# Kernel tuning notes

Measured on AMD Instinct MI355X. Metric: run time of the kernel, lower is better.

## Reference

```python
import jax, jax.numpy as jnp
import numpy as np

NUM_LAYERS = 4
D_MODEL = 1024
N_HEAD = 8
HEAD_DIM = D_MODEL // N_HEAD
FFN_DIM = 4096
B, L = 8, 512
LN_EPS = 1e-5


def rel_pos_embed(seq_len, dim, init_size=1200, padding_idx=0):
    # RelativeSinusoidalPositionalEmbedding.get_embedding(init_size+1, dim, 0)
    num = init_size + 1  # 1201
    half = dim // 2
    inv = np.exp(np.arange(half, dtype=np.float64) * -(np.log(10000.0) / (half - 1)))
    pos = np.arange(-num // 2, num // 2, dtype=np.float64)[:, None] * inv[None, :]
    emb = np.concatenate([np.sin(pos), np.cos(pos)], axis=1)  # [num, dim]
    emb[padding_idx] = 0.0
    origin_shift = num // 2 + 1  # 601
    idx = np.arange(-seq_len, seq_len) + origin_shift  # [2L]
    return jnp.asarray(emb[idx], dtype=jnp.float32)  # [2L, dim]


def _shift(BD):
    # [b,h,L,2L] -> [b,h,L,L], selecting relative offsets k-q
    b, h, l, _ = BD.shape
    BD = jnp.concatenate([BD, jnp.zeros((b, h, l, 1), BD.dtype)], axis=-1)
    BD = BD.reshape(b, h, -1, l)[:, :, :-1].reshape(b, h, l, 2 * l)
    return BD[:, :, :, l:]


def _transpose_shift(E):
    # [b,h,L,2L] -> [b,h,L,L]
    b, h, l, _ = E.shape
    E = jnp.concatenate([E, jnp.zeros((b, h, l, 1), E.dtype)], axis=-1)
    E = E.reshape(b, h, 2 * l + 1, l)
    E = E[:, :, 2 * jnp.arange(l) + 1, :]  # [b,h,L,L]
    return jnp.swapaxes(E, -1, -2)


def layer_norm(x, g, b):
    mu = x.mean(-1, keepdims=True)
    var = ((x - mu) ** 2).mean(-1, keepdims=True)
    return (x - mu) / jnp.sqrt(var + LN_EPS) * g + b


def rel_attn(x, mask, qkv_w, r_r, r_w, pos):
    bsz, l, d = x.shape
    qkv = x @ qkv_w  # [b,L,3D]
    q, k, v = jnp.split(qkv, 3, axis=-1)
    to_heads = lambda t: t.reshape(bsz, l, N_HEAD, HEAD_DIM).transpose(0, 2, 1, 3)
    q, k, v = to_heads(q), to_heads(k), to_heads(v)  # [b,h,L,hd]
    rw_q = q + r_r[:, None]  # (original adds r_r_bias here)
    AC = jnp.einsum('bnqd,bnkd->bnqk', rw_q, k)
    D_ = jnp.einsum('nd,ld->nl', r_w, pos)[None, :, None]   # [1,h,1,2L]
    B_ = jnp.einsum('bnqd,ld->bnql', q, pos)                # [b,h,L,2L]
    E_ = jnp.einsum('bnqd,ld->bnql', k, pos)
    BDE = _shift(B_ + D_) + _transpose_shift(E_)
    attn = AC + BDE  # scale == 1 (scale=False)
    attn = jnp.where(mask[:, None, None, :] == 0, -jnp.inf, attn)
    attn = jax.nn.softmax(attn, axis=-1)
    out = jnp.einsum('bnqk,bnkd->bnqd', attn, v)
    return out.transpose(0, 2, 1, 3).reshape(bsz, l, d)


def setup_inputs() -> dict:
    key = jax.random.key(0)
    ks = jax.random.split(key, 12)
    Ln = NUM_LAYERS
    s = 0.02
    return {
        'x': jax.random.normal(ks[0], (B, L, D_MODEL), jnp.float32),
        'mask': jnp.ones((B, L), jnp.int32),
        'qkv_w': jax.random.normal(ks[1], (Ln, D_MODEL, 3 * D_MODEL), jnp.float32) * s,
        'r_r_bias': jax.random.normal(ks[2], (Ln, N_HEAD, HEAD_DIM), jnp.float32) * s,
        'r_w_bias': jax.random.normal(ks[3], (Ln, N_HEAD, HEAD_DIM), jnp.float32) * s,
        'ln1_g': jnp.ones((Ln, D_MODEL), jnp.float32),
        'ln1_b': jnp.zeros((Ln, D_MODEL), jnp.float32),
        'ln2_g': jnp.ones((Ln, D_MODEL), jnp.float32),
        'ln2_b': jnp.zeros((Ln, D_MODEL), jnp.float32),
        'w1': jax.random.normal(ks[4], (Ln, D_MODEL, FFN_DIM), jnp.float32) * s,
        'b1': jnp.zeros((Ln, FFN_DIM), jnp.float32),
        'w2': jax.random.normal(ks[5], (Ln, FFN_DIM, D_MODEL), jnp.float32) * s,
        'b2': jnp.zeros((Ln, D_MODEL), jnp.float32),
    }


def reference(x, mask, qkv_w, r_r_bias, r_w_bias, ln1_g, ln1_b, ln2_g, ln2_b, w1, b1, w2, b2):
    pos = rel_pos_embed(x.shape[1], HEAD_DIM)  # [2L, hd], buffer (detached)
    for i in range(NUM_LAYERS):  # after_norm=True (post-LN)
        a = rel_attn(x, mask, qkv_w[i], r_r_bias[i], r_w_bias[i], pos)
        x = layer_norm(x + a, ln1_g[i], ln1_b[i])
        h = jax.nn.relu(x @ w1[i] + b1[i]) @ w2[i] + b2[i]
        x = layer_norm(x + h, ln2_g[i], ln2_b[i])
    return x
```

## Files before the change

### kernel.cpp

```cpp
#include <hip/hip_runtime.h>

#define SEQ 512
#define DM 1024
#define NH 8
#define HD 128
#define FFN 4096
#define NL 4
#define NB 8

typedef __attribute__((ext_vector_type(8))) _Float16 half8v;
typedef __attribute__((ext_vector_type(8))) unsigned short ushort8v;
typedef __attribute__((ext_vector_type(4))) float float4v;

__device__ __forceinline__ unsigned short f2h(float f) {
  _Float16 h = (_Float16)f;
  return *(unsigned short*)&h;
}
__device__ __forceinline__ float h2f(unsigned short u) {
  _Float16 h = *(_Float16*)&u;
  return (float)h;
}

__global__ void sc_kernel(float* __restrict__ sc) {
  int idx = blockIdx.x * blockDim.x + threadIdx.x;
  int q = idx >> 6, c = idx & 63;
  if (q >= SEQ) return;
  double a = exp(-(double)c * (9.210340371976184 / 63.0));
  double p = (double)q * a;
  sc[q * 128 + c] = (float)sin(p);
  sc[q * 128 + 64 + c] = (float)cos(p);
}

__global__ void cvt_copy(const float* __restrict__ in, float* __restrict__ xout,
                         unsigned short* __restrict__ xh, int n4) {
  int i = blockIdx.x * blockDim.x + threadIdx.x;
  if (i >= n4) return;
  float4 v = ((const float4*)in)[i];
  ((float4*)xout)[i] = v;
  ushort4 u;
  u.x = f2h(v.x); u.y = f2h(v.y); u.z = f2h(v.z); u.w = f2h(v.w);
  ((ushort4*)xh)[i] = u;
}

__global__ __launch_bounds__(256) void transpose_cvt(
    const float* __restrict__ in, unsigned short* __restrict__ out, int K, int N) {
  __shared__ float t[32][33];
  int n0 = blockIdx.x * 32, k0 = blockIdx.y * 32;
  int c = threadIdx.x & 31, r = threadIdx.x >> 5;
#pragma unroll
  for (int i = 0; i < 32; i += 8)
    t[r + i][c] = in[(long long)(k0 + r + i) * N + n0 + c];
  __syncthreads();
#pragma unroll
  for (int i = 0; i < 32; i += 8)
    out[(long long)(n0 + r + i) * K + k0 + c] = f2h(t[c][r + i]);
}

template<int R, int T>
__device__ __forceinline__ void stage_tile(
    const unsigned short* __restrict__ g, long long ld, int k0,
    unsigned short* lds, int tid) {
#pragma unroll
  for (int i = 0; i < R * 64 / 8 / T; i++) {
    int p = i * T + tid;
    int row = p >> 3, cs = p & 7;
    int c = cs ^ (row & 7);
    const unsigned short* src = g + (long long)row * ld + k0 + c * 8;
    __builtin_amdgcn_global_load_lds(
        (const __attribute__((address_space(1))) void*)src,
        (__attribute__((address_space(3))) void*)(lds + p * 8),
        16, 0, 0);
  }
}

template<int BIAS, int RELU, int OUTH>
__global__ __launch_bounds__(512, 2) void gemm256(
    const unsigned short* __restrict__ A, int lda, long long sAz,
    const unsigned short* __restrict__ Bt, int ldb, long long sBz,
    const float* __restrict__ bias,
    void* __restrict__ Cv, int ldc, long long sCz,
    int K) {
  __shared__ __align__(16) unsigned short As[2][256 * 64];
  __shared__ __align__(16) unsigned short Bs[2][256 * 64];
  const int tid = threadIdx.x, lane = tid & 63, w = tid >> 6;
  const int wm = w >> 2, wn = w & 3;
  const int l15 = lane & 15, l4 = lane >> 4;
  const int gx = gridDim.x, gy = gridDim.y;
  int nwg = gx * gy * gridDim.z;
  int lin = (blockIdx.z * gy + blockIdx.y) * gx + blockIdx.x;
  int swz = (lin & 7) * (nwg >> 3) + (lin >> 3);
  int bx = swz % gx;
  int t2 = swz / gx;
  int by = t2 % gy;
  int z  = t2 / gy;
  const unsigned short* Ag = A + (long long)z * sAz + (long long)by * 256 * lda;
  const unsigned short* Bg = Bt + (long long)z * sBz + (long long)bx * 256 * ldb;

  float4v acc[8][4] = {};
  const int nt = K >> 6;
  stage_tile<256, 512>(Ag, lda, 0, As[0], tid);
  stage_tile<256, 512>(Bg, ldb, 0, Bs[0], tid);
  int cur = 0;
  for (int t = 0; t < nt; t++) {
    if (t + 1 < nt) {
      stage_tile<256, 512>(Ag, lda, (t + 1) << 6, As[cur ^ 1], tid);
      stage_tile<256, 512>(Bg, ldb, (t + 1) << 6, Bs[cur ^ 1], tid);
      asm volatile("s_waitcnt vmcnt(8)" ::: "memory");
    } else {
      asm volatile("s_waitcnt vmcnt(0)" ::: "memory");
    }
    asm volatile("s_barrier" ::: "memory");
#pragma unroll
    for (int ks = 0; ks < 2; ks++) {
      half8v af[8], bf[4];
#pragma unroll
      for (int m = 0; m < 8; m++) {
        int row = wm * 128 + m * 16 + l15;
        int cs = (ks * 4 + l4) ^ (row & 7);
        af[m] = *(const half8v*)&As[cur][row * 64 + cs * 8];
      }
#pragma unroll
      for (int n = 0; n < 4; n++) {
        int row = wn * 64 + n * 16 + l15;
        int cs = (ks * 4 + l4) ^ (row & 7);
        bf[n] = *(const half8v*)&Bs[cur][row * 64 + cs * 8];
      }
#pragma unroll
      for (int m = 0; m < 8; m++)
#pragma unroll
        for (int n = 0; n < 4; n++)
          acc[m][n] = __builtin_amdgcn_mfma_f32_16x16x32_f16(af[m], bf[n], acc[m][n], 0, 0, 0);
    }
    asm volatile("s_barrier" ::: "memory");
    cur ^= 1;
  }
#pragma unroll
  for (int n = 0; n < 4; n++) {
    int ccol = bx * 256 + wn * 64 + n * 16 + l15;
    float bv = BIAS ? bias[ccol] : 0.f;
#pragma unroll
    for (int m = 0; m < 8; m++) {
      int crow0 = by * 256 + wm * 128 + m * 16 + l4 * 4;
#pragma unroll
      for (int j = 0; j < 4; j++) {
        float v = acc[m][n][j] + bv;
        if (RELU) v = fmaxf(v, 0.f);
        long long off = (long long)z * sCz + (long long)(crow0 + j) * ldc + ccol;
        if (OUTH) ((unsigned short*)Cv)[off] = f2h(v);
        else      ((float*)Cv)[off] = v;
      }
    }
  }
}

__global__ __launch_bounds__(256) void build_aug(
    const unsigned short* __restrict__ qkv_h,
    const float* __restrict__ rr, const float* __restrict__ rw,
    const float* __restrict__ sc,
    unsigned short* __restrict__ Ahat, unsigned short* __restrict__ Bhat)
{
  const int z = blockIdx.y, b = z >> 3, h = z & 7;
  const int r = threadIdx.x >> 7, lane = threadIdx.x & 127;
  const int q = blockIdx.x * 2 + r;
  __shared__ float Qf[2][128], Kf[2][128], SC[2][128];
  const unsigned short* row = qkv_h + ((long long)(b * SEQ + q)) * 3072 + h * HD;
  float qv = h2f(row[lane]);
  float kv = h2f(row[DM + lane]);
  Qf[r][lane] = qv + rw[h * HD + lane];
  Kf[r][lane] = kv;
  SC[r][lane] = sc[q * 128 + lane];
  __syncthreads();
  unsigned short* Arow = Ahat + ((long long)z * SEQ + q) * 384;
  unsigned short* Brow = Bhat + ((long long)z * SEQ + q) * 384;
  Arow[lane] = f2h(qv + rr[h * HD + lane]);
  Brow[lane] = f2h(kv);
  if (lane < 64) {
    float S = SC[r][lane], C = SC[r][64 + lane];
    Arow[128 + lane] = f2h(Qf[r][lane] * C + Qf[r][64 + lane] * S);
    Arow[256 + lane] = f2h(S);
    Brow[128 + lane] = f2h(S);
    Brow[256 + lane] = f2h(Kf[r][lane] * C + Kf[r][64 + lane] * S);
  } else {
    int c = lane - 64;
    float S = SC[r][c], C = SC[r][lane];
    Arow[192 + c] = f2h(Qf[r][lane] * C - Qf[r][c] * S);
    Arow[320 + c] = f2h(C);
    Brow[192 + c] = f2h(C);
    Brow[320 + c] = f2h(Kf[r][lane] * C - Kf[r][c] * S);
  }
}

__global__ __launch_bounds__(256) void transpose_v(
    const unsigned short* __restrict__ qkv_h, unsigned short* __restrict__ Vt)
{
  __shared__ unsigned short t[32][33];
  const int z = blockIdx.z, b = z >> 3, h = z & 7;
  const int d0 = blockIdx.x * 32, j0 = blockIdx.y * 32;
  const int c = threadIdx.x & 31, r = threadIdx.x >> 5;
#pragma unroll
  for (int i = 0; i < 32; i += 8)
    t[r + i][c] = qkv_h[((long long)(b * SEQ + j0 + r + i)) * 3072 + 2 * DM + h * HD + d0 + c];
  __syncthreads();
#pragma unroll
  for (int i = 0; i < 32; i += 8)
    Vt[(long long)z * HD * SEQ + (long long)(d0 + r + i) * SEQ + j0 + c] = t[c][r + i];
}

__global__ __launch_bounds__(512, 4) void attn_fused(
    const unsigned short* __restrict__ Ahat,
    const unsigned short* __restrict__ Bhat,
    const unsigned short* __restrict__ Vt,
    const int* __restrict__ mask,
    unsigned short* __restrict__ out)
{
  __shared__ __align__(16) unsigned short S[64 * 512];
  __shared__ __align__(16) unsigned short St[128 * 64];
  const int tid = threadIdx.x, lane = tid & 63, w = tid >> 6;
  const int wr = w >> 1, wc = w & 1;
  const int l15 = lane & 15, l4 = lane >> 4;
  int lin = blockIdx.z * gridDim.x + blockIdx.x;
  int nwg = gridDim.x * gridDim.z;
  int swz = (lin & 7) * (nwg >> 3) + (lin >> 3);
  int qt = swz % gridDim.x, z = swz / gridDim.x;
  const int b = z >> 3, h = z & 7;
  const int q0 = qt * 64;

  half8v qf[12];
  {
    const unsigned short* Ar = Ahat + ((long long)z * SEQ + q0 + wr * 16 + l15) * 384;
#pragma unroll
    for (int k = 0; k < 12; k++)
      qf[k] = *(const half8v*)&Ar[k * 32 + l4 * 8];
  }

  for (int jt = 0; jt < 4; jt++) {
    float4v acc[4] = {};
    const unsigned short* Bg = Bhat + ((long long)z * SEQ + jt * 128) * 384;
    for (int k0 = 0; k0 < 384; k0 += 64) {
      __syncthreads();
      stage_tile<128, 512>(Bg, 384, k0, St, tid);
      __syncthreads();
#pragma unroll
      for (int kk = 0; kk < 2; kk++) {
        int kidx = (k0 >> 5) + kk;
#pragma unroll
        for (int n = 0; n < 4; n++) {
          int row = wc * 64 + n * 16 + l15;
          int cs = (kk * 4 + l4) ^ (row & 7);
          half8v bf = *(const half8v*)&St[row * 64 + cs * 8];
          acc[n] = __builtin_amdgcn_mfma_f32_16x16x32_f16(qf[kidx], bf, acc[n], 0, 0, 0);
        }
      }
    }
#pragma unroll
    for (int n = 0; n < 4; n++) {
      int col = jt * 128 + wc * 64 + n * 16 + l15;
#pragma unroll
      for (int j = 0; j < 4; j++) {
        int row = wr * 16 + l4 * 4 + j;
        int byte = (row * 512 + col) * 2;
        byte ^= (row & 7) << 4;
        *(unsigned short*)((char*)S + byte) = f2h(acc[n][j]);
      }
    }
  }
  __syncthreads();

  float* bias = (float*)St;
  float* Linv = (float*)St + 512;
  if (tid < 128) {
    int4 mk = ((const int4*)(mask + (size_t)b * SEQ))[tid];
    float4 bv;
    bv.x = mk.x ? 0.f : -1e30f;
    bv.y = mk.y ? 0.f : -1e30f;
    bv.z = mk.z ? 0.f : -1e30f;
    bv.w = mk.w ? 0.f : -1e30f;
    ((float4*)bias)[tid] = bv;
  }
  __syncthreads();
  {
    const int row = tid >> 3;
    const int cb = (tid & 7) * 64;
    float mx = -1e30f;
#pragma unroll
    for (int i = 0; i < 8; i++) {
      int byte = (row * 512 + cb + i * 8) * 2;
      byte ^= (row & 7) << 4;
      ushort8v u = *(const ushort8v*)((const char*)S + byte);
      const float* bp = bias + cb + i * 8;
#pragma unroll
      for (int e = 0; e < 8; e++)
        mx = fmaxf(mx, h2f(u[e]) + bp[e]);
    }
    mx = fmaxf(mx, __shfl_xor(mx, 1));
    mx = fmaxf(mx, __shfl_xor(mx, 2));
    mx = fmaxf(mx, __shfl_xor(mx, 4));
    float sum = 0.f;
#pragma unroll
    for (int i = 0; i < 8; i++) {
      int byte = (row * 512 + cb + i * 8) * 2;
      byte ^= (row & 7) << 4;
      ushort8v u = *(const ushort8v*)((const char*)S + byte);
      const float* bp = bias + cb + i * 8;
#pragma unroll
      for (int e = 0; e < 8; e++) {
        float ev = __expf(h2f(u[e]) + bp[e] - mx);
        sum += ev;
        u[e] = f2h(ev);
      }
      *(ushort8v*)((char*)S + byte) = u;
    }
    sum += __shfl_xor(sum, 1);
    sum += __shfl_xor(sum, 2);
    sum += __shfl_xor(sum, 4);
    if ((tid & 7) == 0) Linv[row] = 1.f / sum;
  }
  __syncthreads();
  float rs[4];
#pragma unroll
  for (int j = 0; j < 4; j++) rs[j] = Linv[wr * 16 + l4 * 4 + j];
  __syncthreads();

  float4v oacc[4] = {};
  const unsigned short* Vg = Vt + (long long)z * HD * SEQ;
  for (int k0 = 0; k0 < 512; k0 += 64) {
    __syncthreads();
    stage_tile<128, 512>(Vg, 512, k0, St, tid);
    __syncthreads();
#pragma unroll
    for (int kk = 0; kk < 2; kk++) {
      int prow = wr * 16 + l15;
      int pb = (prow * 512 + k0 + kk * 32 + l4 * 8) * 2;
      pb ^= (prow & 7) << 4;
      half8v af = *(const half8v*)((const char*)S + pb);
#pragma unroll
      for (int n = 0; n < 4; n++) {
        int row = wc * 64 + n * 16 + l15;
        int cs = (kk * 4 + l4) ^ (row & 7);
        half8v bf = *(const half8v*)&St[row * 64 + cs * 8];
        oacc[n] = __builtin_amdgcn_mfma_f32_16x16x32_f16(af, bf, oacc[n], 0, 0, 0);
      }
    }
  }
#pragma unroll
  for (int j = 0; j < 4; j++) {
    int row = q0 + wr * 16 + l4 * 4 + j;
#pragma unroll
    for (int n = 0; n < 4; n++) {
      int col = h * HD + wc * 64 + n * 16 + l15;
      out[((long long)(b * SEQ + row)) * DM + col] = f2h(oacc[n][j] * rs[j]);
    }
  }
}

__global__ __launch_bounds__(256) void add_ln_cvt(
    float* __restrict__ x, const unsigned short* __restrict__ a,
    const float* __restrict__ g, const float* __restrict__ bt,
    unsigned short* __restrict__ xh)
{
  const int row = blockIdx.x, tid = threadIdx.x;
  float4* xp = (float4*)(x + (size_t)row * DM);
  const ushort4 av = ((const ushort4*)(a + (size_t)row * DM))[tid];
  float4 xv = xp[tid];
  float4 s = make_float4(xv.x + h2f(av.x), xv.y + h2f(av.y),
                         xv.z + h2f(av.z), xv.w + h2f(av.w));
  __shared__ float red[4];
  float sum = s.x + s.y + s.z + s.w;
  for (int o = 32; o; o >>= 1) sum += __shfl_down(sum, o);
  if ((tid & 63) == 0) red[tid >> 6] = sum;
  __syncthreads();
  float mu = (red[0] + red[1] + red[2] + red[3]) * (1.f / DM);
  float dx = s.x - mu, dy = s.y - mu, dz = s.z - mu, dw = s.w - mu;
  float sq = dx * dx + dy * dy + dz * dz + dw * dw;
  for (int o = 32; o; o >>= 1) sq += __shfl_down(sq, o);
  __syncthreads();
  if ((tid & 63) == 0) red[tid >> 6] = sq;
  __syncthreads();
  float var = (red[0] + red[1] + red[2] + red[3]) * (1.f / DM);
  float rstd = rsqrtf(var + 1e-5f);
  const float4 gv = ((const float4*)g)[tid];
  const float4 bv = ((const float4*)bt)[tid];
  float4 o4 = make_float4(dx * rstd * gv.x + bv.x, dy * rstd * gv.y + bv.y,
                          dz * rstd * gv.z + bv.z, dw * rstd * gv.w + bv.w);
  xp[tid] = o4;
  ushort4 u;
  u.x = f2h(o4.x); u.y = f2h(o4.y); u.z = f2h(o4.z); u.w = f2h(o4.w);
  ((ushort4*)(xh + (size_t)row * DM))[tid] = u;
}

__global__ __launch_bounds__(256) void add_ln_cvt4(
    float* __restrict__ x, const unsigned short* __restrict__ p, long long pstride,
    const float* __restrict__ bias,
    const float* __restrict__ g, const float* __restrict__ bt,
    unsigned short* __restrict__ xh)
{
  const int row = blockIdx.x, tid = threadIdx.x;
  float4* xp = (float4*)(x + (size_t)row * DM);
  const float4 bb = ((const float4*)bias)[tid];
  float4 xv = xp[tid];
  float4 s = make_float4(xv.x + bb.x, xv.y + bb.y, xv.z + bb.z, xv.w + bb.w);
#pragma unroll
  for (int zz = 0; zz < 4; zz++) {
    const ushort4 a = ((const ushort4*)(p + zz * pstride + (size_t)row * DM))[tid];
    s.x += h2f(a.x); s.y += h2f(a.y); s.z += h2f(a.z); s.w += h2f(a.w);
  }
  __shared__ float red[4];
  float sum = s.x + s.y + s.z + s.w;
  for (int o = 32; o; o >>= 1) sum += __shfl_down(sum, o);
  if ((tid & 63) == 0) red[tid >> 6] = sum;
  __syncthreads();
  float mu = (red[0] + red[1] + red[2] + red[3]) * (1.f / DM);
  float dx = s.x - mu, dy = s.y - mu, dz = s.z - mu, dw = s.w - mu;
  float sq = dx * dx + dy * dy + dz * dz + dw * dw;
  for (int o = 32; o; o >>= 1) sq += __shfl_down(sq, o);
  __syncthreads();
  if ((tid & 63) == 0) red[tid >> 6] = sq;
  __syncthreads();
  float var = (red[0] + red[1] + red[2] + red[3]) * (1.f / DM);
  float rstd = rsqrtf(var + 1e-5f);
  const float4 gv = ((const float4*)g)[tid];
  const float4 bv = ((const float4*)bt)[tid];
  float4 o4 = make_float4(dx * rstd * gv.x + bv.x, dy * rstd * gv.y + bv.y,
                          dz * rstd * gv.z + bv.z, dw * rstd * gv.w + bv.w);
  xp[tid] = o4;
  ushort4 u;
  u.x = f2h(o4.x); u.y = f2h(o4.y); u.z = f2h(o4.z); u.w = f2h(o4.w);
  ((ushort4*)(xh + (size_t)row * DM))[tid] = u;
}

extern "C" void kernel_launch(void* const* d_in, const int* in_sizes, int n_in,
                              void* d_out, int out_size, void* d_ws, size_t ws_size,
                              hipStream_t stream)
{
  const float* x_in = (const float*)d_in[0];
  const int*   mask = (const int*)d_in[1];
  const float* qkv_w = (const float*)d_in[2];
  const float* r_r  = (const float*)d_in[3];
  const float* r_w  = (const float*)d_in[4];
  const float* ln1g = (const float*)d_in[5];
  const float* ln1b = (const float*)d_in[6];
  const float* ln2g = (const float*)d_in[7];
  const float* ln2b = (const float*)d_in[8];
  const float* w1   = (const float*)d_in[9];
  const float* b1   = (const float*)d_in[10];
  const float* w2   = (const float*)d_in[11];
  const float* b2   = (const float*)d_in[12];
  float* x = (float*)d_out;
  char* ws = (char*)d_ws;

  const int ROWS = NB * SEQ;

  const size_t sc_off   = 0;
  const size_t xh_off   = 0x40000;
  const size_t wt_off   = xh_off + (size_t)ROWS * DM * 2;
  const size_t a16_off  = wt_off + (size_t)FFN * DM * 2;
  const size_t qkvh_off = a16_off + (size_t)ROWS * DM * 2;
  const size_t e_off    = qkvh_off + (size_t)ROWS * 3 * DM * 2;

  const size_t ab_bytes = (size_t)64 * SEQ * 384 * 2;
  const size_t hb_bytes = (size_t)ROWS * FFN * 2;
  const size_t part_off = e_off + hb_bytes;

  float* sc     = (float*)(ws + sc_off);
  unsigned short* xh = (unsigned short*)(ws + xh_off);
  unsigned short* wt = (unsigned short*)(ws + wt_off);
  unsigned short* a16 = (unsigned short*)(ws + a16_off);
  unsigned short* qkvh = (unsigned short*)(ws + qkvh_off);
  unsigned short* Ahat = (unsigned short*)(ws + e_off);
  unsigned short* Bhat = (unsigned short*)(ws + e_off + ab_bytes);
  unsigned short* Vt   = (unsigned short*)(ws + e_off + 2 * ab_bytes);
  unsigned short* hb = (unsigned short*)(ws + e_off);
  unsigned short* part = (unsigned short*)(ws + part_off);

  sc_kernel<<<dim3(SEQ * 64 / 256), 256, 0, stream>>>(sc);
  cvt_copy<<<dim3(ROWS * DM / 4 / 256), 256, 0, stream>>>(x_in, x, xh, ROWS * DM / 4);

  for (int L = 0; L < NL; L++) {
    transpose_cvt<<<dim3(3 * DM / 32, DM / 32), 256, 0, stream>>>(
        qkv_w + (size_t)L * DM * 3 * DM, wt, DM, 3 * DM);
    gemm256<0,0,1><<<dim3(3 * DM / 256, ROWS / 256, 1), 512, 0, stream>>>(
        xh, DM, 0, wt, DM, 0, nullptr, qkvh, 3 * DM, 0, DM);

    build_aug<<<dim3(SEQ / 2, 64), 256, 0, stream>>>(
        qkvh, r_r + (size_t)L * NH * HD, r_w + (size_t)L * NH * HD, sc, Ahat, Bhat);
    transpose_v<<<dim3(HD / 32, SEQ / 32, 64), 256, 0, stream>>>(qkvh, Vt);
    attn_fused<<<dim3(SEQ / 64, 1, 64), 512, 0, stream>>>(Ahat, Bhat, Vt, mask, a16);

    add_ln_cvt<<<dim3(ROWS), 256, 0, stream>>>(x, a16, ln1g + (size_t)L * DM, ln1b + (size_t)L * DM, xh);

    transpose_cvt<<<dim3(FFN / 32, DM / 32), 256, 0, stream>>>(
        w1 + (size_t)L * DM * FFN, wt, DM, FFN);
    gemm256<1,1,1><<<dim3(FFN / 256, ROWS / 256, 1), 512, 0, stream>>>(
        xh, DM, 0, wt, DM, 0, b1 + (size_t)L * FFN, hb, FFN, 0, DM);

    transpose_cvt<<<dim3(DM / 32, FFN / 32), 256, 0, stream>>>(
        w2 + (size_t)L * FFN * DM, wt, FFN, DM);
    gemm256<0,0,1><<<dim3(DM / 256, ROWS / 256, 4), 512, 0, stream>>>(
        hb, FFN, 1024, wt, FFN, 1024, nullptr,
        part, DM, (long long)ROWS * DM, 1024);

    add_ln_cvt4<<<dim3(ROWS), 256, 0, stream>>>(
        x, part, (long long)ROWS * DM, b2 + (size_t)L * DM,
        ln2g + (size_t)L * DM, ln2b + (size_t)L * DM, xh);
  }
}
```

Before: 919.2 us.

## Register-prefetch next K/V tile in attention kernel to overlap global loads

Replaces the synchronous global_load_lds staging in the attention kernel's QK and PV loops with a register-staged software pipeline. The next 128x64 tile is loaded into registers while the current one is consumed, and __syncthreads is replaced by raw s_barrier plus explicit lgkmcnt waits. It also raises wave priority around the MFMA blocks and changes the softmax column mapping to interleave threads across columns. This aims to hide global memory latency behind MFMA work, at the cost of extra VGPRs and of relying on hand-placed waitcnts for correctness.

```diff
diff --git a/kernel.cpp b/kernel.cpp
--- a/kernel.cpp
+++ b/kernel.cpp
@@ -71,6 +71,23 @@
         (__attribute__((address_space(3))) void*)(lds + p * 8),
         16, 0, 0);
   }
+}
+
+__device__ __forceinline__ void load_stage128(
+    const unsigned short* __restrict__ g, long long ld, int k0, int tid, ushort8v* v) {
+#pragma unroll
+  for (int i = 0; i < 2; i++) {
+    int p = i * 512 + tid;
+    int row = p >> 3, cs = p & 7;
+    int c = cs ^ (row & 7);
+    v[i] = *(const ushort8v*)(g + (long long)row * ld + k0 + c * 8);
+  }
+}
+__device__ __forceinline__ void write_stage128(
+    unsigned short* St, int tid, const ushort8v* v) {
+#pragma unroll
+  for (int i = 0; i < 2; i++)
+    *(ushort8v*)(St + (i * 512 + tid) * 8) = v[i];
 }
 
 template<int BIAS, int RELU, int OUTH>
@@ -233,16 +250,26 @@
       qf[k] = *(const half8v*)&Ar[k * 32 + l4 * 8];
   }
 
+  ushort8v stg[2];
+  load_stage128(Bhat + ((long long)z * SEQ) * 384, 384, 0, tid, stg);
+#pragma unroll
   for (int jt = 0; jt < 4; jt++) {
     float4v acc[4] = {};
-    const unsigned short* Bg = Bhat + ((long long)z * SEQ + jt * 128) * 384;
-    for (int k0 = 0; k0 < 384; k0 += 64) {
-      __syncthreads();
-      stage_tile<128, 512>(Bg, 384, k0, St, tid);
-      __syncthreads();
+#pragma unroll
+    for (int k6 = 0; k6 < 6; k6++) {
+      __builtin_amdgcn_s_barrier();
+      write_stage128(St, tid, stg);
+      int ns = jt * 6 + k6 + 1;
+      if (ns < 24) {
+        const unsigned short* Bg = Bhat + ((long long)z * SEQ + (ns / 6) * 128) * 384;
+        load_stage128(Bg, 384, (ns % 6) * 64, tid, stg);
+      }
+      asm volatile("s_waitcnt lgkmcnt(0)" ::: "memory");
+      __builtin_amdgcn_s_barrier();
+      __builtin_amdgcn_s_setprio(1);
 #pragma unroll
       for (int kk = 0; kk < 2; kk++) {
-        int kidx = (k0 >> 5) + kk;
+        int kidx = k6 * 2 + kk;
 #pragma unroll
         for (int n = 0; n < 4; n++) {
           int row = wc * 64 + n * 16 + l15;
@@ -251,6 +278,7 @@
           acc[n] = __builtin_amdgcn_mfma_f32_16x16x32_f16(qf[kidx], bf, acc[n], 0, 0, 0);
         }
       }
+      __builtin_amdgcn_s_setprio(0);
     }
 #pragma unroll
     for (int n = 0; n < 4; n++) {
@@ -264,7 +292,12 @@
       }
     }
   }
-  __syncthreads();
+
+  const unsigned short* Vg = Vt + (long long)z * HD * SEQ;
+  load_stage128(Vg, 512, 0, tid, stg);
+
+  asm volatile("s_waitcnt lgkmcnt(0)" ::: "memory");
+  __builtin_amdgcn_s_barrier();
 
   float* bias = (float*)St;
   float* Linv = (float*)St + 512;
@@ -277,17 +310,19 @@
     bv.w = mk.w ? 0.f : -1e30f;
     ((float4*)bias)[tid] = bv;
   }
-  __syncthreads();
+  asm volatile("s_waitcnt lgkmcnt(0)" ::: "memory");
+  __builtin_amdgcn_s_barrier();
   {
     const int row = tid >> 3;
-    const int cb = (tid & 7) * 64;
+    const int c8 = tid & 7;
     float mx = -1e30f;
 #pragma unroll
     for (int i = 0; i < 8; i++) {
-      int byte = (row * 512 + cb + i * 8) * 2;
+      int col = i * 64 + c8 * 8;
+      int byte = (row * 512 + col) * 2;
       byte ^= (row & 7) << 4;
       ushort8v u = *(const ushort8v*)((const char*)S + byte);
-      const float* bp = bias + cb + i * 8;
+      const float* bp = bias + col;
 #pragma unroll
       for (int e = 0; e < 8; e++)
         mx = fmaxf(mx, h2f(u[e]) + bp[e]);
@@ -298,10 +333,11 @@
     float sum = 0.f;
 #pragma unroll
     for (int i = 0; i < 8; i++) {
-      int byte = (row * 512 + cb + i * 8) * 2;
+      int col = i * 64 + c8 * 8;
+      int byte = (row * 512 + col) * 2;
       byte ^= (row & 7) << 4;
       ushort8v u = *(const ushort8v*)((const char*)S + byte);
-      const float* bp = bias + cb + i * 8;
+      const float* bp = bias + col;
 #pragma unroll
       for (int e = 0; e < 8; e++) {
         float ev = __expf(h2f(u[e]) + bp[e] - mx);
@@ -313,24 +349,28 @@
     sum += __shfl_xor(sum, 1);
     sum += __shfl_xor(sum, 2);
     sum += __shfl_xor(sum, 4);
-    if ((tid & 7) == 0) Linv[row] = 1.f / sum;
-  }
-  __syncthreads();
+    if (c8 == 0) Linv[row] = 1.f / sum;
+  }
+  asm volatile("s_waitcnt lgkmcnt(0)" ::: "memory");
+  __builtin_amdgcn_s_barrier();
   float rs[4];
 #pragma unroll
   for (int j = 0; j < 4; j++) rs[j] = Linv[wr * 16 + l4 * 4 + j];
-  __syncthreads();
+  asm volatile("s_waitcnt lgkmcnt(0)" ::: "memory");
 
   float4v oacc[4] = {};
-  const unsigned short* Vg = Vt + (long long)z * HD * SEQ;
-  for (int k0 = 0; k0 < 512; k0 += 64) {
-    __syncthreads();
-    stage_tile<128, 512>(Vg, 512, k0, St, tid);
-    __syncthreads();
+#pragma unroll
+  for (int k8 = 0; k8 < 8; k8++) {
+    __builtin_amdgcn_s_barrier();
+    write_stage128(St, tid, stg);
+    if (k8 + 1 < 8) load_stage128(Vg, 512, (k8 + 1) * 64, tid, stg);
+    asm volatile("s_waitcnt lgkmcnt(0)" ::: "memory");
+    __builtin_amdgcn_s_barrier();
+    __builtin_amdgcn_s_setprio(1);
 #pragma unroll
     for (int kk = 0; kk < 2; kk++) {
       int prow = wr * 16 + l15;
-      int pb = (prow * 512 + k0 + kk * 32 + l4 * 8) * 2;
+      int pb = (prow * 512 + k8 * 64 + kk * 32 + l4 * 8) * 2;
       pb ^= (prow & 7) << 4;
       half8v af = *(const half8v*)((const char*)S + pb);
 #pragma unroll
@@ -341,6 +381,7 @@
         oacc[n] = __builtin_amdgcn_mfma_f32_16x16x32_f16(af, bf, oacc[n], 0, 0, 0);
       }
     }
+    __builtin_amdgcn_s_setprio(0);
   }
 #pragma unroll
   for (int j = 0; j < 4; j++) {
```

After: 863.9 us. 6.0% less time.
